# Optimization experiments

Hardware: AMD Instinct MI355X
Metric: run time of the kernel (lower is better)

The kernel has to match this reference:

```python
import jax, jax.numpy as jnp
import numpy as np

EPS = 1e-5

def _point_batch_norm(x, gamma, beta):
    # BatchNorm1d over channel dim of (B, N, C): stats over (B, N), biased var (training mode)
    mu = jnp.mean(x, axis=(0, 1))
    var = jnp.var(x, axis=(0, 1))
    return (x - mu) * jax.lax.rsqrt(var + EPS) * gamma + beta

def setup_inputs() -> dict:
    key = jax.random.key(0)
    ks = jax.random.split(key, 10)
    B, M, N, K = 4, 16384, 32768, 16
    C, Cs, O = 64, 64, 64
    curr_coords = jax.random.normal(ks[0], (B, M, 3), jnp.float32)
    curr_feat = jax.random.normal(ks[1], (B, M, C), jnp.float32)
    skip_coords = jax.random.normal(ks[2], (B, N, 3), jnp.float32)
    skip_feat = jax.random.normal(ks[3], (B, N, Cs), jnp.float32)
    upsampling_idxs = jax.random.randint(ks[4], (B, N, K), 0, M, jnp.int64)
    s1 = 1.0 / np.sqrt(C)
    s2 = 1.0 / np.sqrt(Cs)
    W1 = jax.random.uniform(ks[5], (C, O), jnp.float32, -s1, s1)
    b1 = jax.random.uniform(ks[6], (O,), jnp.float32, -s1, s1)
    W2 = jax.random.uniform(ks[7], (Cs, O), jnp.float32, -s2, s2)
    b2 = jax.random.uniform(ks[8], (O,), jnp.float32, -s2, s2)
    g1 = jnp.ones((O,), jnp.float32); beta1 = jnp.zeros((O,), jnp.float32)
    g2 = jnp.ones((O,), jnp.float32); beta2 = jnp.zeros((O,), jnp.float32)
    return {
        "curr_coords": curr_coords, "curr_feat": curr_feat,
        "skip_coords": skip_coords, "skip_feat": skip_feat,
        "upsampling_idxs": upsampling_idxs,
        "W1": W1, "b1": b1, "g1": g1, "beta1": beta1,
        "W2": W2, "b2": b2, "g2": g2, "beta2": beta2,
    }

def reference(curr_coords, curr_feat, skip_coords, skip_feat, upsampling_idxs,
              W1, b1, g1, beta1, W2, b2, g2, beta2):
    # Gather K-NN neighbor features per skip point: (B, N, K, C), then max over K
    gathered = jax.vmap(lambda f, i: f[i])(curr_feat, upsampling_idxs)
    pooled = jnp.max(gathered, axis=2)  # (B, N, C)
    # proj: Linear -> PointBatchNorm -> ReLU
    h = jax.nn.relu(_point_batch_norm(pooled @ W1 + b1, g1, beta1))
    # proj_skip on skip features
    hs = jax.nn.relu(_point_batch_norm(skip_feat @ W2 + b2, g2, beta2))
    return jnp.concatenate([skip_coords, h, hs], axis=-1)  # (B, N, 3 + 2*O)
```

## Files before the change

### kernel.cpp

```cpp
#include <hip/hip_runtime.h>

#define BB 4
#define MM 16384
#define NN 32768
#define KK 16
#define ROWS (BB * NN)
#define OUTW 131
#define TROWS 16
#define A_BLOCKS (ROWS / (TROWS * 4))
#define APAD 72


typedef _Float16 half8  __attribute__((ext_vector_type(8)));
typedef _Float16 half2v __attribute__((ext_vector_type(2)));
typedef float f32x4 __attribute__((ext_vector_type(4)));

#define MFMA16(a, b, c) __builtin_amdgcn_mfma_f32_16x16x32_f16(a, b, c, 0, 0, 0)

__device__ __forceinline__ half8 load_bfrag(const float* __restrict__ W, int lane, int ot, int kt) {
    const int kb  = kt * 32 + ((lane >> 4) << 3);
    const int col = ot * 16 + (lane & 15);
    half8 b;
#pragma unroll
    for (int j = 0; j < 8; ++j) b[j] = (_Float16)W[(kb + j) * 64 + col];
    return b;
}

__device__ __forceinline__ half2v gpair(const float* __restrict__ cfb, int mi, int pb, int coff) {
    float q0x = -3.402823466e38f, q0y = q0x, q1x = q0x, q1y = q0x;
#pragma unroll
    for (int k = 0; k < KK; k += 2) {
        const int m0 = __builtin_amdgcn_ds_bpermute(pb + (k << 2), mi);
        const int m1 = __builtin_amdgcn_ds_bpermute(pb + ((k + 1) << 2), mi);
        const float2 v0 = *(const float2*)&cfb[((size_t)m0 << 6) + coff];
        const float2 v1 = *(const float2*)&cfb[((size_t)m1 << 6) + coff];
        q0x = fmaxf(q0x, v0.x); q0y = fmaxf(q0y, v0.y);
        q1x = fmaxf(q1x, v1.x); q1y = fmaxf(q1y, v1.y);
    }
    half2v h;
    h[0] = (_Float16)fmaxf(q0x, q1x);
    h[1] = (_Float16)fmaxf(q0y, q1y);
    return h;
}

__global__ __launch_bounds__(256) void k_pool_proj(
    const float* __restrict__ cf, const int* __restrict__ idxs,
    const float* __restrict__ scoord,
    const float* __restrict__ W1, const float* __restrict__ b1,
    float* __restrict__ out, float* __restrict__ acc)
{
    __shared__ _Float16 ah[4][TROWS][APAD];
    __shared__ float lsum[64], lsq[64];
    const int lane = threadIdx.x & 63;
    const int wv   = threadIdx.x >> 6;
    if (threadIdx.x < 64) { lsum[threadIdx.x] = 0.f; lsq[threadIdx.x] = 0.f; }
    __syncthreads();

    const int w     = blockIdx.x;
    const int xcd   = w & 7;
    const int batch = xcd >> 1;
    const int lb    = (w >> 3) + ((xcd & 1) << 8);
    const int rbase = batch * NN + (lb * 4 + wv) * TROWS;
    const float* cfb = cf + ((size_t)batch << 20);

    const half8 b00 = load_bfrag(W1, lane, 0, 0), b01 = load_bfrag(W1, lane, 0, 1);
    const half8 b10 = load_bfrag(W1, lane, 1, 0), b11 = load_bfrag(W1, lane, 1, 1);
    const half8 b20 = load_bfrag(W1, lane, 2, 0), b21 = load_bfrag(W1, lane, 2, 1);
    const half8 b30 = load_bfrag(W1, lane, 3, 0), b31 = load_bfrag(W1, lane, 3, 1);
    const float bias0 = b1[(lane & 15) +  0], bias1 = b1[(lane & 15) + 16];
    const float bias2 = b1[(lane & 15) + 32], bias3 = b1[(lane & 15) + 48];

    const int mi0 = idxs[(size_t)(rbase +  0) * KK + lane];
    const int mi1 = idxs[(size_t)(rbase +  4) * KK + lane];
    const int mi2 = idxs[(size_t)(rbase +  8) * KK + lane];
    const int mi3 = idxs[(size_t)(rbase + 12) * KK + lane];

    if (lane < 48) {
        const float cv = scoord[(size_t)rbase * 3 + lane];
        const int rr = lane / 3;
        out[(size_t)(rbase + rr) * OUTW + (lane - rr * 3)] = cv;
    }

    const int rr   = lane >> 5;
    const int coff = (lane & 31) << 1;
    const int pb0  = (0 + rr) << 6;
    const int pb2  = (2 + rr) << 6;

    *(half2v*)&ah[wv][ 0 + rr][coff] = gpair(cfb, mi0, pb0, coff);
    *(half2v*)&ah[wv][ 2 + rr][coff] = gpair(cfb, mi0, pb2, coff);
    *(half2v*)&ah[wv][ 4 + rr][coff] = gpair(cfb, mi1, pb0, coff);
    *(half2v*)&ah[wv][ 6 + rr][coff] = gpair(cfb, mi1, pb2, coff);
    *(half2v*)&ah[wv][ 8 + rr][coff] = gpair(cfb, mi2, pb0, coff);
    *(half2v*)&ah[wv][10 + rr][coff] = gpair(cfb, mi2, pb2, coff);
    *(half2v*)&ah[wv][12 + rr][coff] = gpair(cfb, mi3, pb0, coff);
    *(half2v*)&ah[wv][14 + rr][coff] = gpair(cfb, mi3, pb2, coff);
    __builtin_amdgcn_wave_barrier();

    const half8 a0 = *(const half8*)&ah[wv][lane & 15][((lane >> 4) << 3)];
    const half8 a1 = *(const half8*)&ah[wv][lane & 15][32 + ((lane >> 4) << 3)];

    f32x4 ac0 = {0.f, 0.f, 0.f, 0.f}, ac1 = ac0, ac2 = ac0, ac3 = ac0;
    ac0 = MFMA16(a0, b00, ac0); ac0 = MFMA16(a1, b01, ac0);
    ac1 = MFMA16(a0, b10, ac1); ac1 = MFMA16(a1, b11, ac1);
    ac2 = MFMA16(a0, b20, ac2); ac2 = MFMA16(a1, b21, ac2);
    ac3 = MFMA16(a0, b30, ac3); ac3 = MFMA16(a1, b31, ac3);
    __builtin_amdgcn_wave_barrier();

    float ps0 = 0.f, ps1 = 0.f, ps2 = 0.f, ps3 = 0.f;
    float pq0 = 0.f, pq1 = 0.f, pq2 = 0.f, pq3 = 0.f;
    const int rl = rbase + ((lane >> 4) << 2);
    const int cl = lane & 15;
#pragma unroll
    for (int j = 0; j < 4; ++j) {
        const size_t ob = (size_t)(rl + j) * OUTW + 3 + cl;
        const float y0 = ac0[j] + bias0;
        const float y1 = ac1[j] + bias1;
        const float y2 = ac2[j] + bias2;
        const float y3 = ac3[j] + bias3;
        out[ob +  0] = y0;
        out[ob + 16] = y1;
        out[ob + 32] = y2;
        out[ob + 48] = y3;
        ps0 += y0; pq0 += y0 * y0;
        ps1 += y1; pq1 += y1 * y1;
        ps2 += y2; pq2 += y2 * y2;
        ps3 += y3; pq3 += y3 * y3;
    }

    atomicAdd(&lsum[cl +  0], ps0); atomicAdd(&lsq[cl +  0], pq0);
    atomicAdd(&lsum[cl + 16], ps1); atomicAdd(&lsq[cl + 16], pq1);
    atomicAdd(&lsum[cl + 32], ps2); atomicAdd(&lsq[cl + 32], pq2);
    atomicAdd(&lsum[cl + 48], ps3); atomicAdd(&lsq[cl + 48], pq3);
    __syncthreads();
    if (threadIdx.x < 64) {
        atomicAdd(&acc[threadIdx.x],      lsum[threadIdx.x]);
        atomicAdd(&acc[64 + threadIdx.x], lsq[threadIdx.x]);
    }
}

__global__ __launch_bounds__(256) void k_skip_proj(
    const float* __restrict__ sf,
    const float* __restrict__ W2, const float* __restrict__ b2,
    float* __restrict__ out, float* __restrict__ acc)
{
    __shared__ float lsum[64], lsq[64];
    const int lane = threadIdx.x & 63;
    const int wv   = threadIdx.x >> 6;
    if (threadIdx.x < 64) { lsum[threadIdx.x] = 0.f; lsq[threadIdx.x] = 0.f; }
    __syncthreads();

    const int tb = (blockIdx.x * 4 + wv) * TROWS;

    const half8 b00 = load_bfrag(W2, lane, 0, 0), b01 = load_bfrag(W2, lane, 0, 1);
    const half8 b10 = load_bfrag(W2, lane, 1, 0), b11 = load_bfrag(W2, lane, 1, 1);
    const half8 b20 = load_bfrag(W2, lane, 2, 0), b21 = load_bfrag(W2, lane, 2, 1);
    const half8 b30 = load_bfrag(W2, lane, 3, 0), b31 = load_bfrag(W2, lane, 3, 1);
    const float bias0 = b2[(lane & 15) +  0], bias1 = b2[(lane & 15) + 16];
    const float bias2 = b2[(lane & 15) + 32], bias3 = b2[(lane & 15) + 48];

    const size_t ab = (size_t)(tb + (lane & 15)) * 64 + ((lane >> 4) << 3);
    const float4 f0 = *(const float4*)&sf[ab +  0];
    const float4 f1 = *(const float4*)&sf[ab +  4];
    const float4 f2 = *(const float4*)&sf[ab + 32];
    const float4 f3 = *(const float4*)&sf[ab + 36];
    const half8 a0 = {(_Float16)f0.x, (_Float16)f0.y, (_Float16)f0.z, (_Float16)f0.w,
                      (_Float16)f1.x, (_Float16)f1.y, (_Float16)f1.z, (_Float16)f1.w};
    const half8 a1 = {(_Float16)f2.x, (_Float16)f2.y, (_Float16)f2.z, (_Float16)f2.w,
                      (_Float16)f3.x, (_Float16)f3.y, (_Float16)f3.z, (_Float16)f3.w};

    f32x4 ac0 = {0.f, 0.f, 0.f, 0.f}, ac1 = ac0, ac2 = ac0, ac3 = ac0;
    ac0 = MFMA16(a0, b00, ac0); ac0 = MFMA16(a1, b01, ac0);
    ac1 = MFMA16(a0, b10, ac1); ac1 = MFMA16(a1, b11, ac1);
    ac2 = MFMA16(a0, b20, ac2); ac2 = MFMA16(a1, b21, ac2);
    ac3 = MFMA16(a0, b30, ac3); ac3 = MFMA16(a1, b31, ac3);

    float ps0 = 0.f, ps1 = 0.f, ps2 = 0.f, ps3 = 0.f;
    float pq0 = 0.f, pq1 = 0.f, pq2 = 0.f, pq3 = 0.f;
    const int rl = tb + ((lane >> 4) << 2);
    const int cl = lane & 15;
#pragma unroll
    for (int j = 0; j < 4; ++j) {
        const size_t ob = (size_t)(rl + j) * OUTW + 67 + cl;
        const float y0 = ac0[j] + bias0;
        const float y1 = ac1[j] + bias1;
        const float y2 = ac2[j] + bias2;
        const float y3 = ac3[j] + bias3;
        out[ob +  0] = y0;
        out[ob + 16] = y1;
        out[ob + 32] = y2;
        out[ob + 48] = y3;
        ps0 += y0; pq0 += y0 * y0;
        ps1 += y1; pq1 += y1 * y1;
        ps2 += y2; pq2 += y2 * y2;
        ps3 += y3; pq3 += y3 * y3;
    }

    atomicAdd(&lsum[cl +  0], ps0); atomicAdd(&lsq[cl +  0], pq0);
    atomicAdd(&lsum[cl + 16], ps1); atomicAdd(&lsq[cl + 16], pq1);
    atomicAdd(&lsum[cl + 32], ps2); atomicAdd(&lsq[cl + 32], pq2);
    atomicAdd(&lsum[cl + 48], ps3); atomicAdd(&lsq[cl + 48], pq3);
    __syncthreads();
    if (threadIdx.x < 64) {
        atomicAdd(&acc[128 + threadIdx.x], lsum[threadIdx.x]);
        atomicAdd(&acc[192 + threadIdx.x], lsq[threadIdx.x]);
    }
}

__global__ void k_stats(float* __restrict__ ws,
                        const float* __restrict__ g1, const float* __restrict__ be1,
                        const float* __restrict__ g2, const float* __restrict__ be2)
{
    const int o = threadIdx.x;
    const float inv = 1.0f / (float)ROWS;
    float m1 = ws[o] * inv;
    float v1 = ws[64 + o] * inv - m1 * m1;
    float a1 = g1[o] * rsqrtf(v1 + 1e-5f);
    ws[256 + o] = a1;
    ws[384 + o] = be1[o] - m1 * a1;
    float m2 = ws[128 + o] * inv;
    float v2 = ws[192 + o] * inv - m2 * m2;
    float a2 = g2[o] * rsqrtf(v2 + 1e-5f);
    ws[256 + 64 + o] = a2;
    ws[384 + 64 + o] = be2[o] - m2 * a2;
}

__global__ __launch_bounds__(256) void k_finalize(float* __restrict__ out,
                                                  const float* __restrict__ ws)
{
    const size_t T  = (size_t)gridDim.x * blockDim.x;
    const size_t t0 = (size_t)blockIdx.x * blockDim.x + threadIdx.x;
#pragma unroll
    for (int i = 0; i < 4; ++i) {
        const size_t e = t0 + (size_t)i * T;
        const size_t r = e >> 7;
        const int    j = (int)(e & 127);
        const size_t ad = r * OUTW + 3 + j;
        const float v = out[ad];
        out[ad] = fmaxf(fmaf(v, ws[256 + j], ws[384 + j]), 0.f);
    }
}

extern "C" void kernel_launch(void* const* d_in, const int* in_sizes, int n_in,
                              void* d_out, int out_size, void* d_ws, size_t ws_size,
                              hipStream_t stream)
{
    const float* cf     = (const float*)d_in[1];
    const float* scoord = (const float*)d_in[2];
    const float* sf     = (const float*)d_in[3];
    const int*   idxs   = (const int*)  d_in[4];
    const float* W1     = (const float*)d_in[5];
    const float* b1     = (const float*)d_in[6];
    const float* g1     = (const float*)d_in[7];
    const float* be1    = (const float*)d_in[8];
    const float* W2     = (const float*)d_in[9];
    const float* b2     = (const float*)d_in[10];
    const float* g2     = (const float*)d_in[11];
    const float* be2    = (const float*)d_in[12];
    float* out = (float*)d_out;
    float* ws  = (float*)d_ws;

    hipMemsetAsync(ws, 0, 256 * sizeof(float), stream);
    k_pool_proj<<<A_BLOCKS, 256, 0, stream>>>(cf, idxs, scoord, W1, b1, out, ws);
    k_skip_proj<<<A_BLOCKS, 256, 0, stream>>>(sf, W2, b2, out, ws);
    k_stats<<<1, 64, 0, stream>>>(ws, g1, be1, g2, be2);
    k_finalize<<<16384, 256, 0, stream>>>(out, ws);
}
```

Baseline: 293.4 us.

## Pre-convert current features to fp16 and gather with packed half max

Adds a pre-pass that converts curr_feat to fp16 into workspace memory. The pooling kernel then gathers 16-bit features with 8-byte loads per lane and reduces them with v_pk_max_f16, halving the bytes moved by the random-index gather. The fp32 path is kept as a fallback when the workspace is too small. The cost is an extra conversion pass over curr_feat (read 16 MB, write 8 MB) each call. Taking the max in fp16 rather than fp32 gives the same result, since rounding to fp16 preserves order.

```diff
diff --git a/kernel.cpp b/kernel.cpp
--- a/kernel.cpp
+++ b/kernel.cpp
@@ -9,13 +9,20 @@
 #define TROWS 16
 #define A_BLOCKS (ROWS / (TROWS * 4))
 #define APAD 72
-
-
-typedef _Float16 half8  __attribute__((ext_vector_type(8)));
-typedef _Float16 half2v __attribute__((ext_vector_type(2)));
+#define CFH_BYTES ((size_t)BB * MM * 64 * 2)
+
+
+typedef _Float16 half8 __attribute__((ext_vector_type(8)));
+typedef _Float16 h2    __attribute__((ext_vector_type(2)));
 typedef float f32x4 __attribute__((ext_vector_type(4)));
 
 #define MFMA16(a, b, c) __builtin_amdgcn_mfma_f32_16x16x32_f16(a, b, c, 0, 0, 0)
+
+__device__ __forceinline__ unsigned pkmax(unsigned a, unsigned b) {
+    unsigned r;
+    asm("v_pk_max_f16 %0, %1, %2" : "=v"(r) : "v"(a), "v"(b));
+    return r;
+}
 
 __device__ __forceinline__ half8 load_bfrag(const float* __restrict__ W, int lane, int ot, int kt) {
     const int kb  = kt * 32 + ((lane >> 4) << 3);
@@ -26,25 +33,19 @@
     return b;
 }
 
-__device__ __forceinline__ half2v gpair(const float* __restrict__ cfb, int mi, int pb, int coff) {
-    float q0x = -3.402823466e38f, q0y = q0x, q1x = q0x, q1y = q0x;
-#pragma unroll
-    for (int k = 0; k < KK; k += 2) {
-        const int m0 = __builtin_amdgcn_ds_bpermute(pb + (k << 2), mi);
-        const int m1 = __builtin_amdgcn_ds_bpermute(pb + ((k + 1) << 2), mi);
-        const float2 v0 = *(const float2*)&cfb[((size_t)m0 << 6) + coff];
-        const float2 v1 = *(const float2*)&cfb[((size_t)m1 << 6) + coff];
-        q0x = fmaxf(q0x, v0.x); q0y = fmaxf(q0y, v0.y);
-        q1x = fmaxf(q1x, v1.x); q1y = fmaxf(q1y, v1.y);
-    }
-    half2v h;
-    h[0] = (_Float16)fmaxf(q0x, q1x);
-    h[1] = (_Float16)fmaxf(q0y, q1y);
-    return h;
-}
-
-__global__ __launch_bounds__(256) void k_pool_proj(
-    const float* __restrict__ cf, const int* __restrict__ idxs,
+__global__ __launch_bounds__(256) void k_half(const float* __restrict__ cf,
+                                              _Float16* __restrict__ cfh)
+{
+    const int i = blockIdx.x * 256 + threadIdx.x;
+    const float4 v = ((const float4*)cf)[i];
+    union { h2 h[2]; float2 f; } u;
+    u.h[0] = h2{(_Float16)v.x, (_Float16)v.y};
+    u.h[1] = h2{(_Float16)v.z, (_Float16)v.w};
+    ((float2*)cfh)[i] = u.f;
+}
+
+__global__ __launch_bounds__(256) void k_pool_proj_h(
+    const _Float16* __restrict__ cfh, const int* __restrict__ idxs,
     const float* __restrict__ scoord,
     const float* __restrict__ W1, const float* __restrict__ b1,
     float* __restrict__ out, float* __restrict__ acc)
@@ -61,7 +62,7 @@
     const int batch = xcd >> 1;
     const int lb    = (w >> 3) + ((xcd & 1) << 8);
     const int rbase = batch * NN + (lb * 4 + wv) * TROWS;
-    const float* cfb = cf + ((size_t)batch << 20);
+    const _Float16* cfb = cfh + ((size_t)batch << 20);
 
     const half8 b00 = load_bfrag(W1, lane, 0, 0), b01 = load_bfrag(W1, lane, 0, 1);
     const half8 b10 = load_bfrag(W1, lane, 1, 0), b11 = load_bfrag(W1, lane, 1, 1);
@@ -77,23 +78,34 @@
 
     if (lane < 48) {
         const float cv = scoord[(size_t)rbase * 3 + lane];
-        const int rr = lane / 3;
-        out[(size_t)(rbase + rr) * OUTW + (lane - rr * 3)] = cv;
-    }
-
-    const int rr   = lane >> 5;
-    const int coff = (lane & 31) << 1;
-    const int pb0  = (0 + rr) << 6;
-    const int pb2  = (2 + rr) << 6;
-
-    *(half2v*)&ah[wv][ 0 + rr][coff] = gpair(cfb, mi0, pb0, coff);
-    *(half2v*)&ah[wv][ 2 + rr][coff] = gpair(cfb, mi0, pb2, coff);
-    *(half2v*)&ah[wv][ 4 + rr][coff] = gpair(cfb, mi1, pb0, coff);
-    *(half2v*)&ah[wv][ 6 + rr][coff] = gpair(cfb, mi1, pb2, coff);
-    *(half2v*)&ah[wv][ 8 + rr][coff] = gpair(cfb, mi2, pb0, coff);
-    *(half2v*)&ah[wv][10 + rr][coff] = gpair(cfb, mi2, pb2, coff);
-    *(half2v*)&ah[wv][12 + rr][coff] = gpair(cfb, mi3, pb0, coff);
-    *(half2v*)&ah[wv][14 + rr][coff] = gpair(cfb, mi3, pb2, coff);
+        const int rj = lane / 3;
+        out[(size_t)(rbase + rj) * OUTW + (lane - rj * 3)] = cv;
+    }
+
+    const int rr = lane >> 4;
+    const int qc = (lane & 15) << 2;
+    const int pb = rr << 6;
+
+#define GATHER_G(mi, g) do {                                                   \
+        const int m0 = __builtin_amdgcn_ds_bpermute(pb, mi);                   \
+        uint2 u0 = *(const uint2*)&cfb[((size_t)m0 << 6) + qc];                \
+        unsigned alo = u0.x, ahi = u0.y;                                       \
+        _Pragma("unroll")                                                      \
+        for (int k = 1; k < KK; ++k) {                                         \
+            const int mk = __builtin_amdgcn_ds_bpermute(pb + (k << 2), mi);    \
+            uint2 uk = *(const uint2*)&cfb[((size_t)mk << 6) + qc];            \
+            alo = pkmax(alo, uk.x);                                            \
+            ahi = pkmax(ahi, uk.y);                                            \
+        }                                                                      \
+        *(unsigned*)&ah[wv][(g << 2) + rr][qc]     = alo;                      \
+        *(unsigned*)&ah[wv][(g << 2) + rr][qc + 2] = ahi;                      \
+    } while (0)
+
+    GATHER_G(mi0, 0);
+    GATHER_G(mi1, 1);
+    GATHER_G(mi2, 2);
+    GATHER_G(mi3, 3);
+#undef GATHER_G
     __builtin_amdgcn_wave_barrier();
 
     const half8 a0 = *(const half8*)&ah[wv][lane & 15][((lane >> 4) << 3)];
@@ -138,6 +150,118 @@
     }
 }
 
+__device__ __forceinline__ h2 gpair(const float* __restrict__ cfb, int mi, int pb, int coff) {
+    float q0x = -3.402823466e38f, q0y = q0x, q1x = q0x, q1y = q0x;
+#pragma unroll
+    for (int k = 0; k < KK; k += 2) {
+        const int m0 = __builtin_amdgcn_ds_bpermute(pb + (k << 2), mi);
+        const int m1 = __builtin_amdgcn_ds_bpermute(pb + ((k + 1) << 2), mi);
+        const float2 v0 = *(const float2*)&cfb[((size_t)m0 << 6) + coff];
+        const float2 v1 = *(const float2*)&cfb[((size_t)m1 << 6) + coff];
+        q0x = fmaxf(q0x, v0.x); q0y = fmaxf(q0y, v0.y);
+        q1x = fmaxf(q1x, v1.x); q1y = fmaxf(q1y, v1.y);
+    }
+    h2 h;
+    h[0] = (_Float16)fmaxf(q0x, q1x);
+    h[1] = (_Float16)fmaxf(q0y, q1y);
+    return h;
+}
+
+__global__ __launch_bounds__(256) void k_pool_proj_f32(
+    const float* __restrict__ cf, const int* __restrict__ idxs,
+    const float* __restrict__ scoord,
+    const float* __restrict__ W1, const float* __restrict__ b1,
+    float* __restrict__ out, float* __restrict__ acc)
+{
+    __shared__ _Float16 ah[4][TROWS][APAD];
+    __shared__ float lsum[64], lsq[64];
+    const int lane = threadIdx.x & 63;
+    const int wv   = threadIdx.x >> 6;
+    if (threadIdx.x < 64) { lsum[threadIdx.x] = 0.f; lsq[threadIdx.x] = 0.f; }
+    __syncthreads();
+
+    const int w     = blockIdx.x;
+    const int xcd   = w & 7;
+    const int batch = xcd >> 1;
+    const int lb    = (w >> 3) + ((xcd & 1) << 8);
+    const int rbase = batch * NN + (lb * 4 + wv) * TROWS;
+    const float* cfb = cf + ((size_t)batch << 20);
+
+    const half8 b00 = load_bfrag(W1, lane, 0, 0), b01 = load_bfrag(W1, lane, 0, 1);
+    const half8 b10 = load_bfrag(W1, lane, 1, 0), b11 = load_bfrag(W1, lane, 1, 1);
+    const half8 b20 = load_bfrag(W1, lane, 2, 0), b21 = load_bfrag(W1, lane, 2, 1);
+    const half8 b30 = load_bfrag(W1, lane, 3, 0), b31 = load_bfrag(W1, lane, 3, 1);
+    const float bias0 = b1[(lane & 15) +  0], bias1 = b1[(lane & 15) + 16];
+    const float bias2 = b1[(lane & 15) + 32], bias3 = b1[(lane & 15) + 48];
+
+    const int mi0 = idxs[(size_t)(rbase +  0) * KK + lane];
+    const int mi1 = idxs[(size_t)(rbase +  4) * KK + lane];
+    const int mi2 = idxs[(size_t)(rbase +  8) * KK + lane];
+    const int mi3 = idxs[(size_t)(rbase + 12) * KK + lane];
+
+    if (lane < 48) {
+        const float cv = scoord[(size_t)rbase * 3 + lane];
+        const int rj = lane / 3;
+        out[(size_t)(rbase + rj) * OUTW + (lane - rj * 3)] = cv;
+    }
+
+    const int rr   = lane >> 5;
+    const int coff = (lane & 31) << 1;
+    const int pb0  = (0 + rr) << 6;
+    const int pb2  = (2 + rr) << 6;
+
+    *(h2*)&ah[wv][ 0 + rr][coff] = gpair(cfb, mi0, pb0, coff);
+    *(h2*)&ah[wv][ 2 + rr][coff] = gpair(cfb, mi0, pb2, coff);
+    *(h2*)&ah[wv][ 4 + rr][coff] = gpair(cfb, mi1, pb0, coff);
+    *(h2*)&ah[wv][ 6 + rr][coff] = gpair(cfb, mi1, pb2, coff);
+    *(h2*)&ah[wv][ 8 + rr][coff] = gpair(cfb, mi2, pb0, coff);
+    *(h2*)&ah[wv][10 + rr][coff] = gpair(cfb, mi2, pb2, coff);
+    *(h2*)&ah[wv][12 + rr][coff] = gpair(cfb, mi3, pb0, coff);
+    *(h2*)&ah[wv][14 + rr][coff] = gpair(cfb, mi3, pb2, coff);
+    __builtin_amdgcn_wave_barrier();
+
+    const half8 a0 = *(const half8*)&ah[wv][lane & 15][((lane >> 4) << 3)];
+    const half8 a1 = *(const half8*)&ah[wv][lane & 15][32 + ((lane >> 4) << 3)];
+
+    f32x4 ac0 = {0.f, 0.f, 0.f, 0.f}, ac1 = ac0, ac2 = ac0, ac3 = ac0;
+    ac0 = MFMA16(a0, b00, ac0); ac0 = MFMA16(a1, b01, ac0);
+    ac1 = MFMA16(a0, b10, ac1); ac1 = MFMA16(a1, b11, ac1);
+    ac2 = MFMA16(a0, b20, ac2); ac2 = MFMA16(a1, b21, ac2);
+    ac3 = MFMA16(a0, b30, ac3); ac3 = MFMA16(a1, b31, ac3);
+    __builtin_amdgcn_wave_barrier();
+
+    float ps0 = 0.f, ps1 = 0.f, ps2 = 0.f, ps3 = 0.f;
+    float pq0 = 0.f, pq1 = 0.f, pq2 = 0.f, pq3 = 0.f;
+    const int rl = rbase + ((lane >> 4) << 2);
+    const int cl = lane & 15;
+#pragma unroll
+    for (int j = 0; j < 4; ++j) {
+        const size_t ob = (size_t)(rl + j) * OUTW + 3 + cl;
+        const float y0 = ac0[j] + bias0;
+        const float y1 = ac1[j] + bias1;
+        const float y2 = ac2[j] + bias2;
+        const float y3 = ac3[j] + bias3;
+        out[ob +  0] = y0;
+        out[ob + 16] = y1;
+        out[ob + 32] = y2;
+        out[ob + 48] = y3;
+        ps0 += y0; pq0 += y0 * y0;
+        ps1 += y1; pq1 += y1 * y1;
+        ps2 += y2; pq2 += y2 * y2;
+        ps3 += y3; pq3 += y3 * y3;
+    }
+
+    atomicAdd(&lsum[cl +  0], ps0); atomicAdd(&lsq[cl +  0], pq0);
+    atomicAdd(&lsum[cl + 16], ps1); atomicAdd(&lsq[cl + 16], pq1);
+    atomicAdd(&lsum[cl + 32], ps2); atomicAdd(&lsq[cl + 32], pq2);
+    atomicAdd(&lsum[cl + 48], ps3); atomicAdd(&lsq[cl + 48], pq3);
+    __syncthreads();
+    if (threadIdx.x < 64) {
+        atomicAdd(&acc[threadIdx.x],      lsum[threadIdx.x]);
+        atomicAdd(&acc[64 + threadIdx.x], lsq[threadIdx.x]);
+    }
+}
+
 __global__ __launch_bounds__(256) void k_skip_proj(
     const float* __restrict__ sf,
     const float* __restrict__ W2, const float* __restrict__ b2,
@@ -259,8 +383,15 @@
     float* out = (float*)d_out;
     float* ws  = (float*)d_ws;
 
-    hipMemsetAsync(ws, 0, 256 * sizeof(float), stream);
-    k_pool_proj<<<A_BLOCKS, 256, 0, stream>>>(cf, idxs, scoord, W1, b1, out, ws);
+    (void)hipMemsetAsync(ws, 0, 2048, stream);
+
+    if (ws_size >= 2048 + CFH_BYTES) {
+        _Float16* cfh = (_Float16*)((char*)ws + 2048);
+        k_half<<<4096, 256, 0, stream>>>(cf, cfh);
+        k_pool_proj_h<<<A_BLOCKS, 256, 0, stream>>>(cfh, idxs, scoord, W1, b1, out, ws);
+    } else {
+        k_pool_proj_f32<<<A_BLOCKS, 256, 0, stream>>>(cf, idxs, scoord, W1, b1, out, ws);
+    }
     k_skip_proj<<<A_BLOCKS, 256, 0, stream>>>(sf, W2, b2, out, ws);
     k_stats<<<1, 64, 0, stream>>>(ws, g1, be1, g2, be2);
     k_finalize<<<16384, 256, 0, stream>>>(out, ws);
```

Result: faster. 275.2 us (-6.2%).

## Merge pool and skip projections into one launch, fold stats into vectorized finalize

Applied to the files above, without the earlier changes.

The pool projection and skip projection kernels become one launch, with blocks split by index: the first 2048 blocks do gather-max and projection, the last 512 do the skip projection with four tiles per wave. The separate stats kernel is removed, and each finalize block recomputes the BN scale and shift into shared memory. The finalize pass now walks the output as float4s, works out column positions with a divide by 131, and passes the coordinate columns through unchanged. This cuts launches and gaps between kernels and vectorizes the finalize traffic, at the cost of redundant per-block stats work and modulo arithmetic in the finalize loop.

```diff
diff --git a/kernel.cpp b/kernel.cpp
--- a/kernel.cpp
+++ b/kernel.cpp
@@ -7,12 +7,15 @@
 #define ROWS (BB * NN)
 #define OUTW 131
 #define TROWS 16
-#define A_BLOCKS (ROWS / (TROWS * 4))
+#define POOL_BLOCKS 2048
+#define SKIP_BLOCKS 512
+#define PROJ_BLOCKS (POOL_BLOCKS + SKIP_BLOCKS)
 #define APAD 72
-
-
-typedef _Float16 half8  __attribute__((ext_vector_type(8)));
-typedef _Float16 half2v __attribute__((ext_vector_type(2)));
+#define FIN_BLOCKS 2096
+
+
+typedef _Float16 half8 __attribute__((ext_vector_type(8)));
+typedef _Float16 h2    __attribute__((ext_vector_type(2)));
 typedef float f32x4 __attribute__((ext_vector_type(4)));
 
 #define MFMA16(a, b, c) __builtin_amdgcn_mfma_f32_16x16x32_f16(a, b, c, 0, 0, 0)
@@ -26,7 +29,7 @@
     return b;
 }
 
-__device__ __forceinline__ half2v gpair(const float* __restrict__ cfb, int mi, int pb, int coff) {
+__device__ __forceinline__ h2 gpair(const float* __restrict__ cfb, int mi, int pb, int coff) {
     float q0x = -3.402823466e38f, q0y = q0x, q1x = q0x, q1y = q0x;
 #pragma unroll
     for (int k = 0; k < KK; k += 2) {
@@ -37,206 +40,206 @@
         q0x = fmaxf(q0x, v0.x); q0y = fmaxf(q0y, v0.y);
         q1x = fmaxf(q1x, v1.x); q1y = fmaxf(q1y, v1.y);
     }
-    half2v h;
+    h2 h;
     h[0] = (_Float16)fmaxf(q0x, q1x);
     h[1] = (_Float16)fmaxf(q0y, q1y);
     return h;
 }
 
-__global__ __launch_bounds__(256) void k_pool_proj(
+__global__ __launch_bounds__(256) void k_proj(
     const float* __restrict__ cf, const int* __restrict__ idxs,
-    const float* __restrict__ scoord,
+    const float* __restrict__ scoord, const float* __restrict__ sf,
     const float* __restrict__ W1, const float* __restrict__ b1,
-    float* __restrict__ out, float* __restrict__ acc)
+    const float* __restrict__ W2, const float* __restrict__ b2,
+    float* __restrict__ out, float* __restrict__ ws)
 {
     __shared__ _Float16 ah[4][TROWS][APAD];
     __shared__ float lsum[64], lsq[64];
     const int lane = threadIdx.x & 63;
     const int wv   = threadIdx.x >> 6;
+    const int cl   = lane & 15;
     if (threadIdx.x < 64) { lsum[threadIdx.x] = 0.f; lsq[threadIdx.x] = 0.f; }
     __syncthreads();
 
-    const int w     = blockIdx.x;
-    const int xcd   = w & 7;
-    const int batch = xcd >> 1;
-    const int lb    = (w >> 3) + ((xcd & 1) << 8);
-    const int rbase = batch * NN + (lb * 4 + wv) * TROWS;
-    const float* cfb = cf + ((size_t)batch << 20);
-
-    const half8 b00 = load_bfrag(W1, lane, 0, 0), b01 = load_bfrag(W1, lane, 0, 1);
-    const half8 b10 = load_bfrag(W1, lane, 1, 0), b11 = load_bfrag(W1, lane, 1, 1);
-    const half8 b20 = load_bfrag(W1, lane, 2, 0), b21 = load_bfrag(W1, lane, 2, 1);
-    const half8 b30 = load_bfrag(W1, lane, 3, 0), b31 = load_bfrag(W1, lane, 3, 1);
-    const float bias0 = b1[(lane & 15) +  0], bias1 = b1[(lane & 15) + 16];
-    const float bias2 = b1[(lane & 15) + 32], bias3 = b1[(lane & 15) + 48];
-
-    const int mi0 = idxs[(size_t)(rbase +  0) * KK + lane];
-    const int mi1 = idxs[(size_t)(rbase +  4) * KK + lane];
-    const int mi2 = idxs[(size_t)(rbase +  8) * KK + lane];
-    const int mi3 = idxs[(size_t)(rbase + 12) * KK + lane];
-
-    if (lane < 48) {
-        const float cv = scoord[(size_t)rbase * 3 + lane];
-        const int rr = lane / 3;
-        out[(size_t)(rbase + rr) * OUTW + (lane - rr * 3)] = cv;
-    }
-
-    const int rr   = lane >> 5;
-    const int coff = (lane & 31) << 1;
-    const int pb0  = (0 + rr) << 6;
-    const int pb2  = (2 + rr) << 6;
-
-    *(half2v*)&ah[wv][ 0 + rr][coff] = gpair(cfb, mi0, pb0, coff);
-    *(half2v*)&ah[wv][ 2 + rr][coff] = gpair(cfb, mi0, pb2, coff);
-    *(half2v*)&ah[wv][ 4 + rr][coff] = gpair(cfb, mi1, pb0, coff);
-    *(half2v*)&ah[wv][ 6 + rr][coff] = gpair(cfb, mi1, pb2, coff);
-    *(half2v*)&ah[wv][ 8 + rr][coff] = gpair(cfb, mi2, pb0, coff);
-    *(half2v*)&ah[wv][10 + rr][coff] = gpair(cfb, mi2, pb2, coff);
-    *(half2v*)&ah[wv][12 + rr][coff] = gpair(cfb, mi3, pb0, coff);
-    *(half2v*)&ah[wv][14 + rr][coff] = gpair(cfb, mi3, pb2, coff);
-    __builtin_amdgcn_wave_barrier();
-
-    const half8 a0 = *(const half8*)&ah[wv][lane & 15][((lane >> 4) << 3)];
-    const half8 a1 = *(const half8*)&ah[wv][lane & 15][32 + ((lane >> 4) << 3)];
-
-    f32x4 ac0 = {0.f, 0.f, 0.f, 0.f}, ac1 = ac0, ac2 = ac0, ac3 = ac0;
-    ac0 = MFMA16(a0, b00, ac0); ac0 = MFMA16(a1, b01, ac0);
-    ac1 = MFMA16(a0, b10, ac1); ac1 = MFMA16(a1, b11, ac1);
-    ac2 = MFMA16(a0, b20, ac2); ac2 = MFMA16(a1, b21, ac2);
-    ac3 = MFMA16(a0, b30, ac3); ac3 = MFMA16(a1, b31, ac3);
-    __builtin_amdgcn_wave_barrier();
-
-    float ps0 = 0.f, ps1 = 0.f, ps2 = 0.f, ps3 = 0.f;
-    float pq0 = 0.f, pq1 = 0.f, pq2 = 0.f, pq3 = 0.f;
-    const int rl = rbase + ((lane >> 4) << 2);
-    const int cl = lane & 15;
-#pragma unroll
-    for (int j = 0; j < 4; ++j) {
-        const size_t ob = (size_t)(rl + j) * OUTW + 3 + cl;
-        const float y0 = ac0[j] + bias0;
-        const float y1 = ac1[j] + bias1;
-        const float y2 = ac2[j] + bias2;
-        const float y3 = ac3[j] + bias3;
-        out[ob +  0] = y0;
-        out[ob + 16] = y1;
-        out[ob + 32] = y2;
-        out[ob + 48] = y3;
-        ps0 += y0; pq0 += y0 * y0;
-        ps1 += y1; pq1 += y1 * y1;
-        ps2 += y2; pq2 += y2 * y2;
-        ps3 += y3; pq3 += y3 * y3;
-    }
-
-    atomicAdd(&lsum[cl +  0], ps0); atomicAdd(&lsq[cl +  0], pq0);
-    atomicAdd(&lsum[cl + 16], ps1); atomicAdd(&lsq[cl + 16], pq1);
-    atomicAdd(&lsum[cl + 32], ps2); atomicAdd(&lsq[cl + 32], pq2);
-    atomicAdd(&lsum[cl + 48], ps3); atomicAdd(&lsq[cl + 48], pq3);
+    if (blockIdx.x < POOL_BLOCKS) {
+        const int w     = blockIdx.x;
+        const int xcd   = w & 7;
+        const int batch = xcd >> 1;
+        const int lb    = (w >> 3) + ((xcd & 1) << 8);
+        const int rbase = batch * NN + (lb * 4 + wv) * TROWS;
+        const float* cfb = cf + ((size_t)batch << 20);
+
+        const half8 b00 = load_bfrag(W1, lane, 0, 0), b01 = load_bfrag(W1, lane, 0, 1);
+        const half8 b10 = load_bfrag(W1, lane, 1, 0), b11 = load_bfrag(W1, lane, 1, 1);
+        const half8 b20 = load_bfrag(W1, lane, 2, 0), b21 = load_bfrag(W1, lane, 2, 1);
+        const half8 b30 = load_bfrag(W1, lane, 3, 0), b31 = load_bfrag(W1, lane, 3, 1);
+        const float bias0 = b1[cl +  0], bias1 = b1[cl + 16];
+        const float bias2 = b1[cl + 32], bias3 = b1[cl + 48];
+
+        const int mi0 = idxs[(size_t)(rbase +  0) * KK + lane];
+        const int mi1 = idxs[(size_t)(rbase +  4) * KK + lane];
+        const int mi2 = idxs[(size_t)(rbase +  8) * KK + lane];
+        const int mi3 = idxs[(size_t)(rbase + 12) * KK + lane];
+
+        if (lane < 48) {
+            const float cv = scoord[(size_t)rbase * 3 + lane];
+            const int rj = lane / 3;
+            out[(size_t)(rbase + rj) * OUTW + (lane - rj * 3)] = cv;
+        }
+
+        const int rr   = lane >> 5;
+        const int coff = (lane & 31) << 1;
+        const int pb0  = (0 + rr) << 6;
+        const int pb2  = (2 + rr) << 6;
+
+        *(h2*)&ah[wv][ 0 + rr][coff] = gpair(cfb, mi0, pb0, coff);
+        *(h2*)&ah[wv][ 2 + rr][coff] = gpair(cfb, mi0, pb2, coff);
+        *(h2*)&ah[wv][ 4 + rr][coff] = gpair(cfb, mi1, pb0, coff);
+        *(h2*)&ah[wv][ 6 + rr][coff] = gpair(cfb, mi1, pb2, coff);
+        *(h2*)&ah[wv][ 8 + rr][coff] = gpair(cfb, mi2, pb0, coff);
+        *(h2*)&ah[wv][10 + rr][coff] = gpair(cfb, mi2, pb2, coff);
+        *(h2*)&ah[wv][12 + rr][coff] = gpair(cfb, mi3, pb0, coff);
+        *(h2*)&ah[wv][14 + rr][coff] = gpair(cfb, mi3, pb2, coff);
+        __builtin_amdgcn_wave_barrier();
+
+        const half8 a0 = *(const half8*)&ah[wv][cl][((lane >> 4) << 3)];
+        const half8 a1 = *(const half8*)&ah[wv][cl][32 + ((lane >> 4) << 3)];
+
+        f32x4 ac0 = {0.f, 0.f, 0.f, 0.f}, ac1 = ac0, ac2 = ac0, ac3 = ac0;
+        ac0 = MFMA16(a0, b00, ac0); ac0 = MFMA16(a1, b01, ac0);
+        ac1 = MFMA16(a0, b10, ac1); ac1 = MFMA16(a1, b11, ac1);
+        ac2 = MFMA16(a0, b20, ac2); ac2 = MFMA16(a1, b21, ac2);
+        ac3 = MFMA16(a0, b30, ac3); ac3 = MFMA16(a1, b31, ac3);
+        __builtin_amdgcn_wave_barrier();
+
+        float ps0 = 0.f, ps1 = 0.f, ps2 = 0.f, ps3 = 0.f;
+        float pq0 = 0.f, pq1 = 0.f, pq2 = 0.f, pq3 = 0.f;
+        const int rl = rbase + ((lane >> 4) << 2);
+#pragma unroll
+        for (int j = 0; j < 4; ++j) {
+            const size_t ob = (size_t)(rl + j) * OUTW + 3 + cl;
+            const float y0 = ac0[j] + bias0;
+            const float y1 = ac1[j] + bias1;
+            const float y2 = ac2[j] + bias2;
+            const float y3 = ac3[j] + bias3;
+            out[ob +  0] = y0;
+            out[ob + 16] = y1;
+            out[ob + 32] = y2;
+            out[ob + 48] = y3;
+            ps0 += y0; pq0 += y0 * y0;
+            ps1 += y1; pq1 += y1 * y1;
+            ps2 += y2; pq2 += y2 * y2;
+            ps3 += y3; pq3 += y3 * y3;
+        }
+
+        atomicAdd(&lsum[cl +  0], ps0); atomicAdd(&lsq[cl +  0], pq0);
+        atomicAdd(&lsum[cl + 16], ps1); atomicAdd(&lsq[cl + 16], pq1);
+        atomicAdd(&lsum[cl + 32], ps2); atomicAdd(&lsq[cl + 32], pq2);
+        atomicAdd(&lsum[cl + 48], ps3); atomicAdd(&lsq[cl + 48], pq3);
+        __syncthreads();
+        if (threadIdx.x < 64) {
+            atomicAdd(&ws[threadIdx.x],      lsum[threadIdx.x]);
+            atomicAdd(&ws[64 + threadIdx.x], lsq[threadIdx.x]);
+        }
+    } else {
+        const int sb = blockIdx.x - POOL_BLOCKS;
+        const half8 b00 = load_bfrag(W2, lane, 0, 0), b01 = load_bfrag(W2, lane, 0, 1);
+        const half8 b10 = load_bfrag(W2, lane, 1, 0), b11 = load_bfrag(W2, lane, 1, 1);
+        const half8 b20 = load_bfrag(W2, lane, 2, 0), b21 = load_bfrag(W2, lane, 2, 1);
+        const half8 b30 = load_bfrag(W2, lane, 3, 0), b31 = load_bfrag(W2, lane, 3, 1);
+        const float bias0 = b2[cl +  0], bias1 = b2[cl + 16];
+        const float bias2 = b2[cl + 32], bias3 = b2[cl + 48];
+
+        float ps0 = 0.f, ps1 = 0.f, ps2 = 0.f, ps3 = 0.f;
+        float pq0 = 0.f, pq1 = 0.f, pq2 = 0.f, pq3 = 0.f;
+
+        for (int t = 0; t < 4; ++t) {
+            const int tb = (((sb * 4 + wv) << 2) + t) * TROWS;
+            const size_t ab = (size_t)(tb + cl) * 64 + ((lane >> 4) << 3);
+            const float4 e0 = *(const float4*)&sf[ab +  0];
+            const float4 e1 = *(const float4*)&sf[ab +  4];
+            const float4 e2 = *(const float4*)&sf[ab + 32];
+            const float4 e3 = *(const float4*)&sf[ab + 36];
+            const half8 a0 = {(_Float16)e0.x, (_Float16)e0.y, (_Float16)e0.z, (_Float16)e0.w,
+                              (_Float16)e1.x, (_Float16)e1.y, (_Float16)e1.z, (_Float16)e1.w};
+            const half8 a1 = {(_Float16)e2.x, (_Float16)e2.y, (_Float16)e2.z, (_Float16)e2.w,
+                              (_Float16)e3.x, (_Float16)e3.y, (_Float16)e3.z, (_Float16)e3.w};
+
+            f32x4 ac0 = {0.f, 0.f, 0.f, 0.f}, ac1 = ac0, ac2 = ac0, ac3 = ac0;
+            ac0 = MFMA16(a0, b00, ac0); ac0 = MFMA16(a1, b01, ac0);
+            ac1 = MFMA16(a0, b10, ac1); ac1 = MFMA16(a1, b11, ac1);
+            ac2 = MFMA16(a0, b20, ac2); ac2 = MFMA16(a1, b21, ac2);
+            ac3 = MFMA16(a0, b30, ac3); ac3 = MFMA16(a1, b31, ac3);
+
+            const int rl = tb + ((lane >> 4) << 2);
+#pragma unroll
+            for (int j = 0; j < 4; ++j) {
+                const size_t ob = (size_t)(rl + j) * OUTW + 67 + cl;
+                const float y0 = ac0[j] + bias0;
+                const float y1 = ac1[j] + bias1;
+                const float y2 = ac2[j] + bias2;
+                const float y3 = ac3[j] + bias3;
+                out[ob +  0] = y0;
+                out[ob + 16] = y1;
+                out[ob + 32] = y2;
+                out[ob + 48] = y3;
+                ps0 += y0; pq0 += y0 * y0;
+                ps1 += y1; pq1 += y1 * y1;
+                ps2 += y2; pq2 += y2 * y2;
+                ps3 += y3; pq3 += y3 * y3;
+            }
+        }
+
+        atomicAdd(&lsum[cl +  0], ps0); atomicAdd(&lsq[cl +  0], pq0);
+        atomicAdd(&lsum[cl + 16], ps1); atomicAdd(&lsq[cl + 16], pq1);
+        atomicAdd(&lsum[cl + 32], ps2); atomicAdd(&lsq[cl + 32], pq2);
+        atomicAdd(&lsum[cl + 48], ps3); atomicAdd(&lsq[cl + 48], pq3);
+        __syncthreads();
+        if (threadIdx.x < 64) {
+            atomicAdd(&ws[128 + threadIdx.x], lsum[threadIdx.x]);
+            atomicAdd(&ws[192 + threadIdx.x], lsq[threadIdx.x]);
+        }
+    }
+}
+
+__global__ __launch_bounds__(256) void k_fin(
+    float* __restrict__ out, const float* __restrict__ ws,
+    const float* __restrict__ g1, const float* __restrict__ be1,
+    const float* __restrict__ g2, const float* __restrict__ be2)
+{
+    __shared__ float af[128], cf_[128];
+    const int tid = threadIdx.x;
+    if (tid < 64) {
+        const float inv = 1.0f / (float)ROWS;
+        const float m1 = ws[tid] * inv;
+        const float v1 = ws[64 + tid] * inv - m1 * m1;
+        const float a1 = g1[tid] * rsqrtf(v1 + 1e-5f);
+        af[tid]  = a1;
+        cf_[tid] = be1[tid] - m1 * a1;
+        const float m2 = ws[128 + tid] * inv;
+        const float v2 = ws[192 + tid] * inv - m2 * m2;
+        const float a2 = g2[tid] * rsqrtf(v2 + 1e-5f);
+        af[64 + tid]  = a2;
+        cf_[64 + tid] = be2[tid] - m2 * a2;
+    }
     __syncthreads();
-    if (threadIdx.x < 64) {
-        atomicAdd(&acc[threadIdx.x],      lsum[threadIdx.x]);
-        atomicAdd(&acc[64 + threadIdx.x], lsq[threadIdx.x]);
-    }
-}
-
-__global__ __launch_bounds__(256) void k_skip_proj(
-    const float* __restrict__ sf,
-    const float* __restrict__ W2, const float* __restrict__ b2,
-    float* __restrict__ out, float* __restrict__ acc)
-{
-    __shared__ float lsum[64], lsq[64];
-    const int lane = threadIdx.x & 63;
-    const int wv   = threadIdx.x >> 6;
-    if (threadIdx.x < 64) { lsum[threadIdx.x] = 0.f; lsq[threadIdx.x] = 0.f; }
-    __syncthreads();
-
-    const int tb = (blockIdx.x * 4 + wv) * TROWS;
-
-    const half8 b00 = load_bfrag(W2, lane, 0, 0), b01 = load_bfrag(W2, lane, 0, 1);
-    const half8 b10 = load_bfrag(W2, lane, 1, 0), b11 = load_bfrag(W2, lane, 1, 1);
-    const half8 b20 = load_bfrag(W2, lane, 2, 0), b21 = load_bfrag(W2, lane, 2, 1);
-    const half8 b30 = load_bfrag(W2, lane, 3, 0), b31 = load_bfrag(W2, lane, 3, 1);
-    const float bias0 = b2[(lane & 15) +  0], bias1 = b2[(lane & 15) + 16];
-    const float bias2 = b2[(lane & 15) + 32], bias3 = b2[(lane & 15) + 48];
-
-    const size_t ab = (size_t)(tb + (lane & 15)) * 64 + ((lane >> 4) << 3);
-    const float4 f0 = *(const float4*)&sf[ab +  0];
-    const float4 f1 = *(const float4*)&sf[ab +  4];
-    const float4 f2 = *(const float4*)&sf[ab + 32];
-    const float4 f3 = *(const float4*)&sf[ab + 36];
-    const half8 a0 = {(_Float16)f0.x, (_Float16)f0.y, (_Float16)f0.z, (_Float16)f0.w,
-                      (_Float16)f1.x, (_Float16)f1.y, (_Float16)f1.z, (_Float16)f1.w};
-    const half8 a1 = {(_Float16)f2.x, (_Float16)f2.y, (_Float16)f2.z, (_Float16)f2.w,
-                      (_Float16)f3.x, (_Float16)f3.y, (_Float16)f3.z, (_Float16)f3.w};
-
-    f32x4 ac0 = {0.f, 0.f, 0.f, 0.f}, ac1 = ac0, ac2 = ac0, ac3 = ac0;
-    ac0 = MFMA16(a0, b00, ac0); ac0 = MFMA16(a1, b01, ac0);
-    ac1 = MFMA16(a0, b10, ac1); ac1 = MFMA16(a1, b11, ac1);
-    ac2 = MFMA16(a0, b20, ac2); ac2 = MFMA16(a1, b21, ac2);
-    ac3 = MFMA16(a0, b30, ac3); ac3 = MFMA16(a1, b31, ac3);
-
-    float ps0 = 0.f, ps1 = 0.f, ps2 = 0.f, ps3 = 0.f;
-    float pq0 = 0.f, pq1 = 0.f, pq2 = 0.f, pq3 = 0.f;
-    const int rl = tb + ((lane >> 4) << 2);
-    const int cl = lane & 15;
-#pragma unroll
-    for (int j = 0; j < 4; ++j) {
-        const size_t ob = (size_t)(rl + j) * OUTW + 67 + cl;
-        const float y0 = ac0[j] + bias0;
-        const float y1 = ac1[j] + bias1;
-        const float y2 = ac2[j] + bias2;
-        const float y3 = ac3[j] + bias3;
-        out[ob +  0] = y0;
-        out[ob + 16] = y1;
-        out[ob + 32] = y2;
-        out[ob + 48] = y3;
-        ps0 += y0; pq0 += y0 * y0;
-        ps1 += y1; pq1 += y1 * y1;
-        ps2 += y2; pq2 += y2 * y2;
-        ps3 += y3; pq3 += y3 * y3;
-    }
-
-    atomicAdd(&lsum[cl +  0], ps0); atomicAdd(&lsq[cl +  0], pq0);
-    atomicAdd(&lsum[cl + 16], ps1); atomicAdd(&lsq[cl + 16], pq1);
-    atomicAdd(&lsum[cl + 32], ps2); atomicAdd(&lsq[cl + 32], pq2);
-    atomicAdd(&lsum[cl + 48], ps3); atomicAdd(&lsq[cl + 48], pq3);
-    __syncthreads();
-    if (threadIdx.x < 64) {
-        atomicAdd(&acc[128 + threadIdx.x], lsum[threadIdx.x]);
-        atomicAdd(&acc[192 + threadIdx.x], lsq[threadIdx.x]);
-    }
-}
-
-__global__ void k_stats(float* __restrict__ ws,
-                        const float* __restrict__ g1, const float* __restrict__ be1,
-                        const float* __restrict__ g2, const float* __restrict__ be2)
-{
-    const int o = threadIdx.x;
-    const float inv = 1.0f / (float)ROWS;
-    float m1 = ws[o] * inv;
-    float v1 = ws[64 + o] * inv - m1 * m1;
-    float a1 = g1[o] * rsqrtf(v1 + 1e-5f);
-    ws[256 + o] = a1;
-    ws[384 + o] = be1[o] - m1 * a1;
-    float m2 = ws[128 + o] * inv;
-    float v2 = ws[192 + o] * inv - m2 * m2;
-    float a2 = g2[o] * rsqrtf(v2 + 1e-5f);
-    ws[256 + 64 + o] = a2;
-    ws[384 + 64 + o] = be2[o] - m2 * a2;
-}
-
-__global__ __launch_bounds__(256) void k_finalize(float* __restrict__ out,
-                                                  const float* __restrict__ ws)
-{
-    const size_t T  = (size_t)gridDim.x * blockDim.x;
-    const size_t t0 = (size_t)blockIdx.x * blockDim.x + threadIdx.x;
-#pragma unroll
-    for (int i = 0; i < 4; ++i) {
-        const size_t e = t0 + (size_t)i * T;
-        const size_t r = e >> 7;
-        const int    j = (int)(e & 127);
-        const size_t ad = r * OUTW + 3 + j;
-        const float v = out[ad];
-        out[ad] = fmaxf(fmaf(v, ws[256 + j], ws[384 + j]), 0.f);
+
+    float4* o4 = (float4*)out;
+#pragma unroll
+    for (int i = 0; i < 8; ++i) {
+        const unsigned f4 = blockIdx.x * 2048u + (unsigned)i * 256u + tid;
+        float4 v = o4[f4];
+        const unsigned e0 = f4 * 4u;
+        const unsigned r0 = e0 / 131u;
+        int c = (int)(e0 - r0 * 131u);
+        if (c >= 3) v.x = fmaxf(fmaf(v.x, af[c - 3], cf_[c - 3]), 0.f);
+        if (++c == 131) c = 0;
+        if (c >= 3) v.y = fmaxf(fmaf(v.y, af[c - 3], cf_[c - 3]), 0.f);
+        if (++c == 131) c = 0;
+        if (c >= 3) v.z = fmaxf(fmaf(v.z, af[c - 3], cf_[c - 3]), 0.f);
+        if (++c == 131) c = 0;
+        if (c >= 3) v.w = fmaxf(fmaf(v.w, af[c - 3], cf_[c - 3]), 0.f);
+        o4[f4] = v;
     }
 }
 
@@ -259,9 +262,8 @@
     float* out = (float*)d_out;
     float* ws  = (float*)d_ws;
 
-    hipMemsetAsync(ws, 0, 256 * sizeof(float), stream);
-    k_pool_proj<<<A_BLOCKS, 256, 0, stream>>>(cf, idxs, scoord, W1, b1, out, ws);
-    k_skip_proj<<<A_BLOCKS, 256, 0, stream>>>(sf, W2, b2, out, ws);
-    k_stats<<<1, 64, 0, stream>>>(ws, g1, be1, g2, be2);
-    k_finalize<<<16384, 256, 0, stream>>>(out, ws);
-}
+    (void)hipMemsetAsync(ws, 0, 1024, stream);
+    k_proj<<<PROJ_BLOCKS, 256, 0, stream>>>(cf, idxs, scoord, sf,
+                                            W1, b1, W2, b2, out, ws);
+    k_fin<<<FIN_BLOCKS, 256, 0, stream>>>(out, ws, g1, be1, g2, be2);
+}
```

Measured after the change: 245.1 us. 16.5% less time.
